# Performance work log

Hardware: AMD Instinct MI355X
Metric: run time of the kernel (lower is better)

The kernel has to match this reference:

```python
import jax, jax.numpy as jnp
import numpy as np

N_FILTERS = 1024
N_HEADS = 16


def setup_inputs() -> dict:
    key = jax.random.key(0)
    k1, k2, k3 = jax.random.split(key, 3)
    x = jax.random.normal(k1, (8, 1024, N_FILTERS), dtype=jnp.float32)
    # VarianceScaling(0.02) ~ small dense init; 0.02*sqrt(1/fan_in) scale approximated
    w_qkv = jax.random.normal(k2, (N_FILTERS, N_FILTERS * 3), dtype=jnp.float32) * (0.02 / N_FILTERS) ** 0.5
    w_out = jax.random.normal(k3, (N_FILTERS, N_FILTERS), dtype=jnp.float32) * (0.02 / N_FILTERS) ** 0.5
    return {"x": x, "w_qkv": w_qkv, "w_out": w_out}


def reference(x, w_qkv, w_out):
    b, n, c = x.shape
    h = N_HEADS
    d = c // h
    qkv = jnp.einsum('bnc,ce->bne', x, w_qkv)  # [b, n, 3c]
    q, k, v = jnp.split(qkv, 3, axis=-1)
    # b n (h d) -> b h n d
    to_heads = lambda t: t.reshape(b, n, h, d).transpose(0, 2, 1, 3)
    q, k, v = to_heads(q), to_heads(k), to_heads(v)
    scale = jnp.sqrt(jnp.asarray(c, jnp.float32))  # NOTE: sqrt(n_filters), matches source
    attn = jnp.einsum('bhnd,bhmd->bhnm', q, k) / scale
    attn = jax.nn.softmax(attn, axis=-1)
    out = jnp.einsum('bhnm,bhmd->bhnd', attn, v)
    out = out.transpose(0, 2, 1, 3).reshape(b, n, c)  # b h n d -> b n (h d)
    return jnp.einsum('bnc,co->bno', out, w_out)
```

## Files before the change

kernel.cpp:

```cpp
#include <hip/hip_runtime.h>
#include <hip/hip_bf16.h>

typedef __bf16 bf16_t;
typedef __bf16 bf16x8 __attribute__((ext_vector_type(8)));
typedef __bf16 bf16x4 __attribute__((ext_vector_type(4)));
typedef short short4v __attribute__((ext_vector_type(4)));
typedef float f32x4 __attribute__((ext_vector_type(4)));

constexpr int LD = 3072;

#define MFMA_16x16x32(a, b, c) __builtin_amdgcn_mfma_f32_16x16x32_bf16((a), (b), (c), 0, 0, 0)
#define MFMA16(a, b, c) \
  __builtin_amdgcn_mfma_f32_16x16x16bf16_1k((a), (b), (c), 0, 0, 0)

#define GLOAD_LDS16(g, l)                                               \
  __builtin_amdgcn_global_load_lds(                                     \
      (const __attribute__((address_space(1))) void*)(g),               \
      (__attribute__((address_space(3))) void*)(l), 16, 0, 0)

#define TRREAD(dst, addr, imm) \
  asm volatile("ds_read_b64_tr_b16 %0, %1 offset:" imm : "=v"(dst) : "v"(addr))

#define BAR __builtin_amdgcn_s_barrier()
#define LGKM0 do { asm volatile("s_waitcnt lgkmcnt(0)" ::: "memory"); \
                   __builtin_amdgcn_sched_barrier(0); } while (0)

__global__ __launch_bounds__(256) void prep_kernel(
    const float* __restrict__ x, bf16_t* __restrict__ x_b,
    const float* __restrict__ w_qkv, bf16_t* __restrict__ wqT,
    const float* __restrict__ w_out, bf16_t* __restrict__ woT) {
  const int blk = blockIdx.x;
  if (blk < 4096) {
    const int i = blk * 256 + threadIdx.x;
    const float4 a = reinterpret_cast<const float4*>(x)[2 * i];
    const float4 c = reinterpret_cast<const float4*>(x)[2 * i + 1];
    bf16x8 o;
    o[0] = (bf16_t)a.x; o[1] = (bf16_t)a.y; o[2] = (bf16_t)a.z; o[3] = (bf16_t)a.w;
    o[4] = (bf16_t)c.x; o[5] = (bf16_t)c.y; o[6] = (bf16_t)c.z; o[7] = (bf16_t)c.w;
    reinterpret_cast<bf16x8*>(x_b)[i] = o;
    return;
  }
  __shared__ float tile[32][33];
  const float* in; bf16_t* outp; int C, bx, by;
  if (blk < 7168) { const int i = blk - 4096; in = w_qkv; outp = wqT; C = 3072; bx = i % 96; by = i / 96; }
  else            { const int i = blk - 7168; in = w_out; outp = woT; C = 1024; bx = i & 31; by = i >> 5; }
  constexpr int R = 1024;
  const int c0 = bx * 32, r0 = by * 32;
  const int tx = threadIdx.x & 31, ty = threadIdx.x >> 5;
#pragma unroll
  for (int i = 0; i < 32; i += 8)
    tile[ty + i][tx] = in[(size_t)(r0 + ty + i) * C + (c0 + tx)];
  __syncthreads();
#pragma unroll
  for (int i = 0; i < 32; i += 8)
    outp[(size_t)(c0 + ty + i) * R + (r0 + tx)] = (bf16_t)tile[tx][ty + i];
}

__global__ __launch_bounds__(512, 2) void gemm_qkv_256(
    const bf16_t* __restrict__ A, const bf16_t* __restrict__ Bt,
    bf16_t* __restrict__ C, float q_scale) {
  constexpr int K = 1024;
  extern __shared__ char smem[];
  char* asB = smem;
  char* bsB = smem + 65536;

  const int t = threadIdx.x;
  const int lane = t & 63, wave = t >> 6;
  const int l15 = lane & 15, lg = lane >> 4;
  const int wr = wave >> 2, wc = wave & 3;

  const int bid = blockIdx.x;
  const int idx = bid >> 3;
  const int rgrp = (bid >> 1) & 3;
  const int cgrp = bid & 1;
  const int brow = (rgrp * 8 + (idx & 7)) * 256;
  const int bcol = (cgrp * 6 + (idx >> 3)) * 256;

  const int srow = t >> 3;
  const int schk = (t & 7) ^ (srow & 7);
  const bf16_t* aS = A + (size_t)(brow + srow) * K + schk * 8;
  const bf16_t* bS = Bt + (size_t)(bcol + srow) * K + schk * 8;
  const int ldst = t * 8;

#define STG_A(T, H) do {                                                      \
    const bf16_t* _s = aS + (size_t)((H) * 128) * K + (T) * 64;               \
    bf16_t* _d = (bf16_t*)(asB + ((T) & 1) * 32768 + (H) * 16384) + ldst;     \
    GLOAD_LDS16(_s, _d);                                                      \
    GLOAD_LDS16(_s + (size_t)64 * K, _d + 4096);                              \
  } while (0)
#define STG_B(T, H) do {                                                      \
    const bf16_t* _s = bS + (size_t)((H) * 128) * K + (T) * 64;               \
    bf16_t* _d = (bf16_t*)(bsB + ((T) & 1) * 32768 + (H) * 16384) + ldst;     \
    GLOAD_LDS16(_s, _d);                                                      \
    GLOAD_LDS16(_s + (size_t)64 * K, _d + 4096);                              \
  } while (0)

  const int rx = l15 & 7;
  const unsigned c0 = ((unsigned)(lg ^ rx)) << 4;
  const unsigned c1 = ((unsigned)((4 | lg) ^ rx)) << 4;
  const unsigned a_rd = (unsigned)(wr * 16384 + l15 * 128);
  const unsigned b_rd = (unsigned)((wc >> 1) * 16384 + (wc & 1) * 8192 + l15 * 128);

  f32x4 acc[8][4] = {};
  bf16x8 af[4][2], bfr[2][2];

#define RD_AF(BUF, MH) do { _Pragma("unroll")                                 \
    for (int m = 0; m < 4; ++m) {                                             \
      const char* _p = asB + (BUF) * 32768 + a_rd + ((MH) * 4 + m) * 2048;    \
      af[m][0] = *(const bf16x8*)(_p + c0);                                   \
      af[m][1] = *(const bf16x8*)(_p + c1); } } while (0)
#define RD_BF(BUF, NH) do { _Pragma("unroll")                                 \
    for (int n = 0; n < 2; ++n) {                                             \
      const char* _p = bsB + (BUF) * 32768 + b_rd + ((NH) * 2 + n) * 2048;    \
      bfr[n][0] = *(const bf16x8*)(_p + c0);                                  \
      bfr[n][1] = *(const bf16x8*)(_p + c1); } } while (0)
#define MM16(MH, NH) do {                                                     \
    __builtin_amdgcn_s_setprio(1);                                            \
    _Pragma("unroll")                                                         \
    for (int m = 0; m < 4; ++m) { _Pragma("unroll")                           \
      for (int n = 0; n < 2; ++n) {                                           \
        acc[(MH)*4+m][(NH)*2+n] =                                             \
            MFMA_16x16x32(af[m][0], bfr[n][0], acc[(MH)*4+m][(NH)*2+n]);      \
        acc[(MH)*4+m][(NH)*2+n] =                                             \
            MFMA_16x16x32(af[m][1], bfr[n][1], acc[(MH)*4+m][(NH)*2+n]); } }  \
    __builtin_amdgcn_s_setprio(0); } while (0)

  STG_A(0, 0); STG_A(0, 1); STG_B(0, 0); STG_B(0, 1); STG_A(1, 0);
  asm volatile("s_waitcnt vmcnt(2)" ::: "memory");
  BAR;

  for (int i = 0; i < 8; ++i) {
    const int T1 = 2 * i + 1, T2 = 2 * i + 2, T3 = 2 * i + 3;
    const bool pf = (i < 7);
    STG_A(T1, 1);
    RD_AF(0, 0); RD_BF(0, 0);
    BAR; LGKM0; MM16(0, 0); BAR;
    STG_B(T1, 0);
    RD_BF(0, 1);
    BAR; LGKM0; MM16(0, 1); BAR;
    STG_B(T1, 1);
    RD_AF(0, 1);
    BAR; LGKM0; MM16(1, 1); BAR;
    if (pf) STG_A(T2, 0);
    RD_BF(0, 0);
    BAR; LGKM0; MM16(1, 0);
    if (pf) asm volatile("s_waitcnt vmcnt(2)" ::: "memory");
    else    asm volatile("s_waitcnt vmcnt(0)" ::: "memory");
    BAR;
    if (pf) STG_A(T2, 1);
    RD_AF(1, 0); RD_BF(1, 0);
    BAR; LGKM0; MM16(0, 0); BAR;
    if (pf) STG_B(T2, 0);
    RD_BF(1, 1);
    BAR; LGKM0; MM16(0, 1); BAR;
    if (pf) STG_B(T2, 1);
    RD_AF(1, 1);
    BAR; LGKM0; MM16(1, 1); BAR;
    if (pf) STG_A(T3, 0);
    RD_BF(1, 0);
    BAR; LGKM0; MM16(1, 0);
    asm volatile("s_waitcnt vmcnt(2)" ::: "memory");
    BAR;
  }

  const float sc = (bcol < 1024) ? q_scale : 1.0f;
  const int crow0 = brow + wr * 128 + lg * 4;
  const int ccol0 = bcol + wc * 64 + l15;
#pragma unroll
  for (int m = 0; m < 8; ++m)
#pragma unroll
    for (int n = 0; n < 4; ++n)
#pragma unroll
      for (int r = 0; r < 4; ++r)
        C[(size_t)(crow0 + m * 16 + r) * 3072 + ccol0 + n * 16] =
            (bf16_t)(acc[m][n][r] * sc);
#undef STG_A
#undef STG_B
#undef RD_AF
#undef RD_BF
#undef MM16
}

template <typename OutT>
__global__ __launch_bounds__(512, 1) void gemm_bt_128x256(
    const bf16_t* __restrict__ A, const bf16_t* __restrict__ Bt,
    OutT* __restrict__ C, int N, int nrowblk, int q_cols, float q_scale) {
  constexpr int K = 1024;
  extern __shared__ char smem[];
  char* asB = smem;
  char* bsB = smem + 49152;

  const int t = threadIdx.x;
  const int lane = t & 63, wave = t >> 6;
  const int l15 = lane & 15, lg = lane >> 4;
  const int wr = wave >> 2, wc = wave & 3;

  const int cpx = (int)gridDim.x >> 3;
  const int bid = blockIdx.x;
  const int wg = (bid & 7) * cpx + (bid >> 3);
  const int brow = (wg % nrowblk) * 128;
  const int bcol = (wg / nrowblk) * 256;

  const int srow = t >> 3;
  const int schk = (t & 7) ^ (srow & 7);
  const bf16_t* aS = A + (size_t)(brow + srow) * K + schk * 8;
  const bf16_t* bS = Bt + (size_t)(bcol + srow) * K + schk * 8;
  const int ldst = t * 8;

#define STG_A(T, BUF) do {                                               \
    const bf16_t* _s = aS + (T) * 64;                                    \
    bf16_t* _d = (bf16_t*)(asB + (BUF) * 16384) + ldst;                  \
    GLOAD_LDS16(_s, _d);                                                 \
    GLOAD_LDS16(_s + (size_t)64 * K, _d + 4096);                         \
  } while (0)
#define STG_B(T, H, BUF) do {                                            \
    const bf16_t* _s = bS + (size_t)((H) * 128) * K + (T) * 64;          \
    bf16_t* _d = (bf16_t*)(bsB + (BUF) * 32768 + (H) * 16384) + ldst;    \
    GLOAD_LDS16(_s, _d);                                                 \
    GLOAD_LDS16(_s + (size_t)64 * K, _d + 4096);                         \
  } while (0)

  const int rx = l15 & 7;
  const unsigned c0 = ((unsigned)(lg ^ rx)) << 4;
  const unsigned c1 = ((unsigned)((4 | lg) ^ rx)) << 4;
  const unsigned a_rd = (unsigned)(wr * 8192 + l15 * 128);
  const unsigned b_rd = (unsigned)((wc >> 1) * 16384 + (wc & 1) * 8192 + l15 * 128);

  f32x4 acc[4][4] = {};
  bf16x8 af[2][2], bfr[4][2];

#define RD_AF(BUF, MH) do { _Pragma("unroll")                            \
    for (int m = 0; m < 2; ++m) {                                        \
      const char* _p = asB + (BUF) * 16384 + a_rd + ((MH) * 2 + m) * 2048; \
      af[m][0] = *(const bf16x8*)(_p + c0);                              \
      af[m][1] = *(const bf16x8*)(_p + c1); } } while (0)
#define RD_BF(BUF) do { _Pragma("unroll")                                \
    for (int n = 0; n < 4; ++n) {                                        \
      const char* _p = bsB + (BUF) * 32768 + b_rd + n * 2048;            \
      bfr[n][0] = *(const bf16x8*)(_p + c0);                             \
      bfr[n][1] = *(const bf16x8*)(_p + c1); } } while (0)
#define MM(MH) do {                                                      \
    __builtin_amdgcn_s_setprio(1);                                       \
    _Pragma("unroll")                                                    \
    for (int m = 0; m < 2; ++m) { _Pragma("unroll")                      \
      for (int n = 0; n < 4; ++n) {                                      \
        acc[(MH)*2+m][n] =                                               \
            MFMA_16x16x32(af[m][0], bfr[n][0], acc[(MH)*2+m][n]);        \
        acc[(MH)*2+m][n] =                                               \
            MFMA_16x16x32(af[m][1], bfr[n][1], acc[(MH)*2+m][n]); } }    \
    __builtin_amdgcn_s_setprio(0); } while (0)

  STG_A(0, 0); STG_B(0, 0, 0); STG_B(0, 1, 0);
  STG_A(1, 1); STG_B(1, 0, 1); STG_B(1, 1, 1);
  asm volatile("s_waitcnt vmcnt(6)" ::: "memory");
  BAR;

  int bc = 0;
  for (int T = 0; T < 16; ++T) {
    const bool pf = (T + 2 < 16);
    const int bs = (bc >= 1) ? (bc - 1) : 2;
    if (pf) { STG_A(T + 2, bs); STG_B(T + 2, 0, bs); }
    RD_AF(bc, 0);
    RD_BF(bc);
    BAR; LGKM0; MM(0); BAR;
    if (pf) STG_B(T + 2, 1, bs);
    RD_AF(bc, 1);
    BAR; LGKM0; MM(1);
    if (pf) asm volatile("s_waitcnt vmcnt(6)" ::: "memory");
    else    asm volatile("s_waitcnt vmcnt(0)" ::: "memory");
    BAR;
    bc = (bc == 2) ? 0 : bc + 1;
  }

  const float sc = (bcol < q_cols) ? q_scale : 1.0f;
  const int crow0 = brow + wr * 64 + lg * 4;
  const int ccol0 = bcol + wc * 64 + l15;
#pragma unroll
  for (int m = 0; m < 4; ++m)
#pragma unroll
    for (int n = 0; n < 4; ++n)
#pragma unroll
      for (int r = 0; r < 4; ++r)
        C[(size_t)(crow0 + m * 16 + r) * N + ccol0 + n * 16] =
            (OutT)(acc[m][n][r] * sc);
#undef STG_A
#undef STG_B
#undef RD_AF
#undef RD_BF
#undef MM
}

__device__ __forceinline__ unsigned pack_bf16_pair(float a, float b) {
  union { __hip_bfloat162 h; unsigned u; } c;
  c.h = __float22bfloat162_rn(float2{a, b});
  return c.u;
}

__global__ __launch_bounds__(256, 3) void attn_kernel(const bf16_t* __restrict__ qkv,
                                                      bf16_t* __restrict__ ctx) {
  __shared__ bf16_t Ks[2][4096];
  __shared__ bf16_t Vs[2][4096];
  const int tid = threadIdx.x, lane = tid & 63, wave = tid >> 6;
  const int l15 = lane & 15, lg = (lane >> 4) & 3;
  const int flat = blockIdx.x;
  const int xcd = flat & 7, rr = flat >> 3;
  const int qt = rr & 7;
  const int hb = xcd * 16 + (rr >> 3);
  const int h = hb & 15, b = hb >> 4;
  const size_t base = (size_t)b * 1024 * LD;
  const int qbase = qt * 128 + wave * 32;

  bf16x8 qa[2][2];
#pragma unroll
  for (int s = 0; s < 2; s++) {
    const bf16_t* qp = qkv + base + (size_t)(qbase + s * 16 + l15) * LD + h * 64 + lg * 8;
    qa[s][0] = *reinterpret_cast<const bf16x8*>(qp);
    qa[s][1] = *reinterpret_cast<const bf16x8*>(qp + 32);
  }

  const bf16_t* Kb = qkv + base + 1024 + h * 64;
  const bf16_t* Vb = qkv + base + 2048 + h * 64;

  const int krr = lane >> 3;
  const int kcc = (lane & 7) ^ krr;
  const bf16_t* ksrc0 = Kb + (size_t)(wave * 16 + krr) * LD + kcc * 8;
  const bf16_t* ksrc1 = ksrc0 + (size_t)8 * LD;

  const int vd0 = (lane & 1) * 8 + wave * 16;
  const int vkv = ((lane >> 1) & 3) + ((lane >> 3) & 3) * 4 + (lane >> 5) * 16;
  const bf16_t* vsrc0 = Vb + (size_t)vkv * LD + vd0;
  const bf16_t* vsrc1 = vsrc0 + (size_t)32 * LD;

  bf16_t* ksb = &Ks[0][0];
  bf16_t* vsb = &Vs[0][0];
  const char* ksr = (const char*)&Ks[0][0];
  const unsigned vs_byte =
      (unsigned)(size_t)(__attribute__((address_space(3))) void*)(&Vs[0][0]);
  const unsigned tr_lane = vs_byte + lane * 8;

  const int rx7 = l15 & 7;
  const unsigned kb0 = (unsigned)(l15 * 128 + ((lg ^ rx7) << 4));
  const unsigned kb1 = (unsigned)(l15 * 128 + (((4 | lg) ^ rx7) << 4));

  short4v ones4;
#pragma unroll
  for (int j = 0; j < 4; j++) {
    union { bf16_t f; short s; } cu; cu.f = (bf16_t)1.0f;
    ones4[j] = cu.s;
  }

  f32x4 dn[2] = {};
  f32x4 oacc[2][4] = {};

  GLOAD_LDS16(ksrc0, ksb + wave * 1024);
  GLOAD_LDS16(ksrc1, ksb + wave * 1024 + 512);
  GLOAD_LDS16(vsrc0, vsb + wave * 1024);
  GLOAD_LDS16(vsrc1, vsb + wave * 1024 + 512);
  ksrc0 += (size_t)64 * LD; ksrc1 += (size_t)64 * LD;
  vsrc0 += (size_t)64 * LD; vsrc1 += (size_t)64 * LD;
  __syncthreads();

#pragma unroll 4
  for (int t = 0; t < 16; t++) {
    const int cur = t & 1;
    if (t < 15) {
      bf16_t* kd = ksb + (cur ^ 1) * 4096 + wave * 1024;
      bf16_t* vd = vsb + (cur ^ 1) * 4096 + wave * 1024;
      GLOAD_LDS16(ksrc0, kd);
      GLOAD_LDS16(ksrc1, kd + 512);
      GLOAD_LDS16(vsrc0, vd);
      GLOAD_LDS16(vsrc1, vd + 512);
      ksrc0 += (size_t)64 * LD; ksrc1 += (size_t)64 * LD;
      vsrc0 += (size_t)64 * LD; vsrc1 += (size_t)64 * LD;
    }

    f32x4 sacc[2][4] = {};
    const char* kt = ksr + cur * 8192;
    __builtin_amdgcn_s_setprio(1);
#pragma unroll
    for (int tt = 0; tt < 4; tt++) {
      const bf16x8 k0 = *reinterpret_cast<const bf16x8*>(kt + tt * 2048 + kb0);
      const bf16x8 k1 = *reinterpret_cast<const bf16x8*>(kt + tt * 2048 + kb1);
      sacc[0][tt] = MFMA_16x16x32(k0, qa[0][0], sacc[0][tt]);
      sacc[0][tt] = MFMA_16x16x32(k1, qa[0][1], sacc[0][tt]);
      sacc[1][tt] = MFMA_16x16x32(k0, qa[1][0], sacc[1][tt]);
      sacc[1][tt] = MFMA_16x16x32(k1, qa[1][1], sacc[1][tt]);
    }
    __builtin_amdgcn_s_setprio(0);

    const unsigned ta = tr_lane + (unsigned)cur * 8192;
    short4v tl0, th0, tl2, th2, tl4, th4, tl6, th6;
    TRREAD(tl0, ta, "0");    TRREAD(th0, ta, "512");
    TRREAD(tl2, ta, "2048"); TRREAD(th2, ta, "2560");
    TRREAD(tl4, ta, "4096"); TRREAD(th4, ta, "4608");
    TRREAD(tl6, ta, "6144"); TRREAD(th6, ta, "6656");
    __builtin_amdgcn_sched_barrier(0);

    unsigned pu[16];
#pragma unroll
    for (int tt = 0; tt < 4; tt++) {
      const float a0 = __builtin_exp2f(sacc[0][tt][0]);
      const float a1 = __builtin_exp2f(sacc[0][tt][1]);
      const float a2 = __builtin_exp2f(sacc[0][tt][2]);
      const float a3 = __builtin_exp2f(sacc[0][tt][3]);
      pu[(tt >> 1) * 4 + (tt & 1) * 2 + 0] = pack_bf16_pair(a0, a1);
      pu[(tt >> 1) * 4 + (tt & 1) * 2 + 1] = pack_bf16_pair(a2, a3);
      const float b0 = __builtin_exp2f(sacc[1][tt][0]);
      const float b1 = __builtin_exp2f(sacc[1][tt][1]);
      const float b2 = __builtin_exp2f(sacc[1][tt][2]);
      const float b3 = __builtin_exp2f(sacc[1][tt][3]);
      pu[8 + (tt >> 1) * 4 + (tt & 1) * 2 + 0] = pack_bf16_pair(b0, b1);
      pu[8 + (tt >> 1) * 4 + (tt & 1) * 2 + 1] = pack_bf16_pair(b2, b3);
    }
    short4v paL[2][2], paH[2][2];
#pragma unroll
    for (int s = 0; s < 2; s++)
#pragma unroll
      for (int ks = 0; ks < 2; ks++) {
        paL[s][ks] = *reinterpret_cast<short4v*>(&pu[s * 8 + ks * 4]);
        paH[s][ks] = *reinterpret_cast<short4v*>(&pu[s * 8 + ks * 4 + 2]);
      }

#pragma unroll
    for (int s = 0; s < 2; s++)
#pragma unroll
      for (int ks = 0; ks < 2; ks++) {
        dn[s] = MFMA16(paL[s][ks], ones4, dn[s]);
        dn[s] = MFMA16(paH[s][ks], ones4, dn[s]);
      }

    short4v tl1, th1, tl3, th3, tl5, th5, tl7, th7;
    TRREAD(tl1, ta, "1024"); TRREAD(th1, ta, "1536");
    TRREAD(tl3, ta, "3072"); TRREAD(th3, ta, "3584");
    TRREAD(tl5, ta, "5120"); TRREAD(th5, ta, "5632");
    TRREAD(tl7, ta, "7168"); TRREAD(th7, ta, "7680");

    asm volatile("s_waitcnt lgkmcnt(8)" ::: "memory");
    __builtin_amdgcn_sched_barrier(0);
    __builtin_amdgcn_s_setprio(1);
#pragma unroll
    for (int s = 0; s < 2; s++) {
      oacc[s][0] = MFMA16(paL[s][0], tl0, oacc[s][0]);
      oacc[s][0] = MFMA16(paH[s][0], th0, oacc[s][0]);
      oacc[s][1] = MFMA16(paL[s][0], tl2, oacc[s][1]);
      oacc[s][1] = MFMA16(paH[s][0], th2, oacc[s][1]);
      oacc[s][2] = MFMA16(paL[s][0], tl4, oacc[s][2]);
      oacc[s][2] = MFMA16(paH[s][0], th4, oacc[s][2]);
      oacc[s][3] = MFMA16(paL[s][0], tl6, oacc[s][3]);
      oacc[s][3] = MFMA16(paH[s][0], th6, oacc[s][3]);
    }
    __builtin_amdgcn_s_setprio(0);

    asm volatile("s_waitcnt lgkmcnt(0)" ::: "memory");
    __builtin_amdgcn_sched_barrier(0);
    __builtin_amdgcn_s_setprio(1);
#pragma unroll
    for (int s = 0; s < 2; s++) {
      oacc[s][0] = MFMA16(paL[s][1], tl1, oacc[s][0]);
      oacc[s][0] = MFMA16(paH[s][1], th1, oacc[s][0]);
      oacc[s][1] = MFMA16(paL[s][1], tl3, oacc[s][1]);
      oacc[s][1] = MFMA16(paH[s][1], th3, oacc[s][1]);
      oacc[s][2] = MFMA16(paL[s][1], tl5, oacc[s][2]);
      oacc[s][2] = MFMA16(paH[s][1], th5, oacc[s][2]);
      oacc[s][3] = MFMA16(paL[s][1], tl7, oacc[s][3]);
      oacc[s][3] = MFMA16(paH[s][1], th7, oacc[s][3]);
    }
    __builtin_amdgcn_s_setprio(0);

    __syncthreads();
  }

#pragma unroll
  for (int s = 0; s < 2; s++) {
#pragma unroll
    for (int r = 0; r < 4; r++) {
      const float inv = 1.0f / dn[s][r];
      const size_t row = (size_t)(b * 1024 + qbase + s * 16 + lg * 4 + r);
#pragma unroll
      for (int dt = 0; dt < 4; dt++)
        ctx[row * 1024 + h * 64 + dt * 16 + l15] = (bf16_t)(oacc[s][dt][r] * inv);
    }
  }
}

extern "C" void kernel_launch(void* const* d_in, const int* in_sizes, int n_in,
                              void* d_out, int out_size, void* d_ws, size_t ws_size,
                              hipStream_t stream) {
  (void)in_sizes; (void)n_in; (void)out_size; (void)ws_size;
  const float* x = (const float*)d_in[0];
  const float* w_qkv = (const float*)d_in[1];
  const float* w_out = (const float*)d_in[2];
  float* out = (float*)d_out;
  char* ws = (char*)d_ws;

  bf16_t* x_b   = (bf16_t*)(ws);
  bf16_t* qkv_b = (bf16_t*)(ws + (size_t)(16 << 20));
  bf16_t* wqT   = (bf16_t*)(ws + (size_t)(64 << 20));
  bf16_t* woT   = (bf16_t*)(ws + (size_t)(70 << 20));
  bf16_t* ctx_b = (bf16_t*)(ws + (size_t)(72 << 20));

  const float qsc = 0.045084220027780106f;

  prep_kernel<<<8192, 256, 0, stream>>>(x, x_b, w_qkv, wqT, w_out, woT);
  gemm_qkv_256<<<384, 512, 131072, stream>>>(x_b, wqT, qkv_b, qsc);
  attn_kernel<<<1024, 256, 0, stream>>>(qkv_b, ctx_b);
  gemm_bt_128x256<float><<<256, 512, 147456, stream>>>(
      ctx_b, woT, out, 1024, 64, 0, 1.0f);
}
```

Measured before the change: 155.7 us.

## Process two query tiles per attention block to reuse K/V tiles

Each attention workgroup now handles 256 query rows (two 128-row sub-tiles per wave set) instead of 128, so every K/V tile staged in LDS is used for twice as many queries and global K/V traffic halves. The grid shrinks from 1024 to 512 blocks and the launch bound drops to 2 waves per SIMD to make room for the doubled accumulators and Q fragments. All V transpose reads are now issued up front and waited on once. The cost is higher register pressure, lower occupancy and fewer blocks to spread across CUs.

```diff
diff --git a/kernel.cpp b/kernel.cpp
--- a/kernel.cpp
+++ b/kernel.cpp
@@ -296,7 +296,7 @@
   return c.u;
 }
 
-__global__ __launch_bounds__(256, 3) void attn_kernel(const bf16_t* __restrict__ qkv,
+__global__ __launch_bounds__(256, 2) void attn_kernel(const bf16_t* __restrict__ qkv,
                                                       bf16_t* __restrict__ ctx) {
   __shared__ bf16_t Ks[2][4096];
   __shared__ bf16_t Vs[2][4096];
@@ -304,19 +304,22 @@
   const int l15 = lane & 15, lg = (lane >> 4) & 3;
   const int flat = blockIdx.x;
   const int xcd = flat & 7, rr = flat >> 3;
-  const int qt = rr & 7;
-  const int hb = xcd * 16 + (rr >> 3);
+  const int qt2 = rr & 3;
+  const int hb = xcd * 16 + (rr >> 2);
   const int h = hb & 15, b = hb >> 4;
   const size_t base = (size_t)b * 1024 * LD;
-  const int qbase = qt * 128 + wave * 32;
-
-  bf16x8 qa[2][2];
-#pragma unroll
-  for (int s = 0; s < 2; s++) {
-    const bf16_t* qp = qkv + base + (size_t)(qbase + s * 16 + l15) * LD + h * 64 + lg * 8;
-    qa[s][0] = *reinterpret_cast<const bf16x8*>(qp);
-    qa[s][1] = *reinterpret_cast<const bf16x8*>(qp + 32);
-  }
+  const int qbase = qt2 * 256 + wave * 32;
+
+  bf16x8 qa[2][2][2];
+#pragma unroll
+  for (int s2 = 0; s2 < 2; s2++)
+#pragma unroll
+    for (int s = 0; s < 2; s++) {
+      const bf16_t* qp =
+          qkv + base + (size_t)(qbase + s2 * 128 + s * 16 + l15) * LD + h * 64 + lg * 8;
+      qa[s2][s][0] = *reinterpret_cast<const bf16x8*>(qp);
+      qa[s2][s][1] = *reinterpret_cast<const bf16x8*>(qp + 32);
+    }
 
   const bf16_t* Kb = qkv + base + 1024 + h * 64;
   const bf16_t* Vb = qkv + base + 2048 + h * 64;
@@ -349,8 +352,8 @@
     ones4[j] = cu.s;
   }
 
-  f32x4 dn[2] = {};
-  f32x4 oacc[2][4] = {};
+  f32x4 dn[2][2] = {};
+  f32x4 oacc[2][2][4] = {};
 
   GLOAD_LDS16(ksrc0, ksb + wave * 1024);
   GLOAD_LDS16(ksrc1, ksb + wave * 1024 + 512);
@@ -360,7 +363,7 @@
   vsrc0 += (size_t)64 * LD; vsrc1 += (size_t)64 * LD;
   __syncthreads();
 
-#pragma unroll 4
+#pragma unroll 2
   for (int t = 0; t < 16; t++) {
     const int cur = t & 1;
     if (t < 15) {
@@ -374,113 +377,141 @@
       vsrc0 += (size_t)64 * LD; vsrc1 += (size_t)64 * LD;
     }
 
-    f32x4 sacc[2][4] = {};
     const char* kt = ksr + cur * 8192;
+    const unsigned ta = tr_lane + (unsigned)cur * 8192;
+    short4v paL[2][2][2], paH[2][2][2];
+
+    f32x4 sacc0[2][4] = {};
     __builtin_amdgcn_s_setprio(1);
 #pragma unroll
     for (int tt = 0; tt < 4; tt++) {
       const bf16x8 k0 = *reinterpret_cast<const bf16x8*>(kt + tt * 2048 + kb0);
       const bf16x8 k1 = *reinterpret_cast<const bf16x8*>(kt + tt * 2048 + kb1);
-      sacc[0][tt] = MFMA_16x16x32(k0, qa[0][0], sacc[0][tt]);
-      sacc[0][tt] = MFMA_16x16x32(k1, qa[0][1], sacc[0][tt]);
-      sacc[1][tt] = MFMA_16x16x32(k0, qa[1][0], sacc[1][tt]);
-      sacc[1][tt] = MFMA_16x16x32(k1, qa[1][1], sacc[1][tt]);
+      sacc0[0][tt] = MFMA_16x16x32(k0, qa[0][0][0], sacc0[0][tt]);
+      sacc0[0][tt] = MFMA_16x16x32(k1, qa[0][0][1], sacc0[0][tt]);
+      sacc0[1][tt] = MFMA_16x16x32(k0, qa[0][1][0], sacc0[1][tt]);
+      sacc0[1][tt] = MFMA_16x16x32(k1, qa[0][1][1], sacc0[1][tt]);
     }
     __builtin_amdgcn_s_setprio(0);
 
-    const unsigned ta = tr_lane + (unsigned)cur * 8192;
-    short4v tl0, th0, tl2, th2, tl4, th4, tl6, th6;
+    short4v tl0, th0, tl1, th1, tl2, th2, tl3, th3;
+    short4v tl4, th4, tl5, th5, tl6, th6, tl7, th7;
     TRREAD(tl0, ta, "0");    TRREAD(th0, ta, "512");
+    TRREAD(tl1, ta, "1024"); TRREAD(th1, ta, "1536");
     TRREAD(tl2, ta, "2048"); TRREAD(th2, ta, "2560");
+    TRREAD(tl3, ta, "3072"); TRREAD(th3, ta, "3584");
     TRREAD(tl4, ta, "4096"); TRREAD(th4, ta, "4608");
+    TRREAD(tl5, ta, "5120"); TRREAD(th5, ta, "5632");
     TRREAD(tl6, ta, "6144"); TRREAD(th6, ta, "6656");
+    TRREAD(tl7, ta, "7168"); TRREAD(th7, ta, "7680");
     __builtin_amdgcn_sched_barrier(0);
 
-    unsigned pu[16];
+    {
+      unsigned pu[16];
+#pragma unroll
+      for (int tt = 0; tt < 4; tt++) {
+#pragma unroll
+        for (int s = 0; s < 2; s++) {
+          const float p0 = __builtin_exp2f(sacc0[s][tt][0]);
+          const float p1 = __builtin_exp2f(sacc0[s][tt][1]);
+          const float p2 = __builtin_exp2f(sacc0[s][tt][2]);
+          const float p3 = __builtin_exp2f(sacc0[s][tt][3]);
+          pu[s * 8 + (tt >> 1) * 4 + (tt & 1) * 2 + 0] = pack_bf16_pair(p0, p1);
+          pu[s * 8 + (tt >> 1) * 4 + (tt & 1) * 2 + 1] = pack_bf16_pair(p2, p3);
+        }
+      }
+#pragma unroll
+      for (int s = 0; s < 2; s++)
+#pragma unroll
+        for (int ks = 0; ks < 2; ks++) {
+          paL[0][s][ks] = *reinterpret_cast<short4v*>(&pu[s * 8 + ks * 4]);
+          paH[0][s][ks] = *reinterpret_cast<short4v*>(&pu[s * 8 + ks * 4 + 2]);
+          dn[0][s] = MFMA16(paL[0][s][ks], ones4, dn[0][s]);
+          dn[0][s] = MFMA16(paH[0][s][ks], ones4, dn[0][s]);
+        }
+    }
+
+    f32x4 sacc1[2][4] = {};
+    __builtin_amdgcn_s_setprio(1);
 #pragma unroll
     for (int tt = 0; tt < 4; tt++) {
-      const float a0 = __builtin_exp2f(sacc[0][tt][0]);
-      const float a1 = __builtin_exp2f(sacc[0][tt][1]);
-      const float a2 = __builtin_exp2f(sacc[0][tt][2]);
-      const float a3 = __builtin_exp2f(sacc[0][tt][3]);
-      pu[(tt >> 1) * 4 + (tt & 1) * 2 + 0] = pack_bf16_pair(a0, a1);
-      pu[(tt >> 1) * 4 + (tt & 1) * 2 + 1] = pack_bf16_pair(a2, a3);
-      const float b0 = __builtin_exp2f(sacc[1][tt][0]);
-      const float b1 = __builtin_exp2f(sacc[1][tt][1]);
-      const float b2 = __builtin_exp2f(sacc[1][tt][2]);
-      const float b3 = __builtin_exp2f(sacc[1][tt][3]);
-      pu[8 + (tt >> 1) * 4 + (tt & 1) * 2 + 0] = pack_bf16_pair(b0, b1);
-      pu[8 + (tt >> 1) * 4 + (tt & 1) * 2 + 1] = pack_bf16_pair(b2, b3);
-    }
-    short4v paL[2][2], paH[2][2];
-#pragma unroll
-    for (int s = 0; s < 2; s++)
-#pragma unroll
-      for (int ks = 0; ks < 2; ks++) {
-        paL[s][ks] = *reinterpret_cast<short4v*>(&pu[s * 8 + ks * 4]);
-        paH[s][ks] = *reinterpret_cast<short4v*>(&pu[s * 8 + ks * 4 + 2]);
-      }
-
-#pragma unroll
-    for (int s = 0; s < 2; s++)
-#pragma unroll
-      for (int ks = 0; ks < 2; ks++) {
-        dn[s] = MFMA16(paL[s][ks], ones4, dn[s]);
-        dn[s] = MFMA16(paH[s][ks], ones4, dn[s]);
-      }
-
-    short4v tl1, th1, tl3, th3, tl5, th5, tl7, th7;
-    TRREAD(tl1, ta, "1024"); TRREAD(th1, ta, "1536");
-    TRREAD(tl3, ta, "3072"); TRREAD(th3, ta, "3584");
-    TRREAD(tl5, ta, "5120"); TRREAD(th5, ta, "5632");
-    TRREAD(tl7, ta, "7168"); TRREAD(th7, ta, "7680");
-
-    asm volatile("s_waitcnt lgkmcnt(8)" ::: "memory");
-    __builtin_amdgcn_sched_barrier(0);
-    __builtin_amdgcn_s_setprio(1);
-#pragma unroll
-    for (int s = 0; s < 2; s++) {
-      oacc[s][0] = MFMA16(paL[s][0], tl0, oacc[s][0]);
-      oacc[s][0] = MFMA16(paH[s][0], th0, oacc[s][0]);
-      oacc[s][1] = MFMA16(paL[s][0], tl2, oacc[s][1]);
-      oacc[s][1] = MFMA16(paH[s][0], th2, oacc[s][1]);
-      oacc[s][2] = MFMA16(paL[s][0], tl4, oacc[s][2]);
-      oacc[s][2] = MFMA16(paH[s][0], th4, oacc[s][2]);
-      oacc[s][3] = MFMA16(paL[s][0], tl6, oacc[s][3]);
-      oacc[s][3] = MFMA16(paH[s][0], th6, oacc[s][3]);
+      const bf16x8 k0 = *reinterpret_cast<const bf16x8*>(kt + tt * 2048 + kb0);
+      const bf16x8 k1 = *reinterpret_cast<const bf16x8*>(kt + tt * 2048 + kb1);
+      sacc1[0][tt] = MFMA_16x16x32(k0, qa[1][0][0], sacc1[0][tt]);
+      sacc1[0][tt] = MFMA_16x16x32(k1, qa[1][0][1], sacc1[0][tt]);
+      sacc1[1][tt] = MFMA_16x16x32(k0, qa[1][1][0], sacc1[1][tt]);
+      sacc1[1][tt] = MFMA_16x16x32(k1, qa[1][1][1], sacc1[1][tt]);
     }
     __builtin_amdgcn_s_setprio(0);
 
-    asm volatile("s_waitcnt lgkmcnt(0)" ::: "memory");
-    __builtin_amdgcn_sched_barrier(0);
+    {
+      unsigned pu[16];
+#pragma unroll
+      for (int tt = 0; tt < 4; tt++) {
+#pragma unroll
+        for (int s = 0; s < 2; s++) {
+          const float p0 = __builtin_exp2f(sacc1[s][tt][0]);
+          const float p1 = __builtin_exp2f(sacc1[s][tt][1]);
+          const float p2 = __builtin_exp2f(sacc1[s][tt][2]);
+          const float p3 = __builtin_exp2f(sacc1[s][tt][3]);
+          pu[s * 8 + (tt >> 1) * 4 + (tt & 1) * 2 + 0] = pack_bf16_pair(p0, p1);
+          pu[s * 8 + (tt >> 1) * 4 + (tt & 1) * 2 + 1] = pack_bf16_pair(p2, p3);
+        }
+      }
+#pragma unroll
+      for (int s = 0; s < 2; s++)
+#pragma unroll
+        for (int ks = 0; ks < 2; ks++) {
+          paL[1][s][ks] = *reinterpret_cast<short4v*>(&pu[s * 8 + ks * 4]);
+          paH[1][s][ks] = *reinterpret_cast<short4v*>(&pu[s * 8 + ks * 4 + 2]);
+          dn[1][s] = MFMA16(paL[1][s][ks], ones4, dn[1][s]);
+          dn[1][s] = MFMA16(paH[1][s][ks], ones4, dn[1][s]);
+        }
+    }
+
+    LGKM0;
+
     __builtin_amdgcn_s_setprio(1);
 #pragma unroll
-    for (int s = 0; s < 2; s++) {
-      oacc[s][0] = MFMA16(paL[s][1], tl1, oacc[s][0]);
-      oacc[s][0] = MFMA16(paH[s][1], th1, oacc[s][0]);
-      oacc[s][1] = MFMA16(paL[s][1], tl3, oacc[s][1]);
-      oacc[s][1] = MFMA16(paH[s][1], th3, oacc[s][1]);
-      oacc[s][2] = MFMA16(paL[s][1], tl5, oacc[s][2]);
-      oacc[s][2] = MFMA16(paH[s][1], th5, oacc[s][2]);
-      oacc[s][3] = MFMA16(paL[s][1], tl7, oacc[s][3]);
-      oacc[s][3] = MFMA16(paH[s][1], th7, oacc[s][3]);
-    }
+    for (int s2 = 0; s2 < 2; s2++)
+#pragma unroll
+      for (int s = 0; s < 2; s++) {
+        oacc[s2][s][0] = MFMA16(paL[s2][s][0], tl0, oacc[s2][s][0]);
+        oacc[s2][s][0] = MFMA16(paH[s2][s][0], th0, oacc[s2][s][0]);
+        oacc[s2][s][0] = MFMA16(paL[s2][s][1], tl1, oacc[s2][s][0]);
+        oacc[s2][s][0] = MFMA16(paH[s2][s][1], th1, oacc[s2][s][0]);
+        oacc[s2][s][1] = MFMA16(paL[s2][s][0], tl2, oacc[s2][s][1]);
+        oacc[s2][s][1] = MFMA16(paH[s2][s][0], th2, oacc[s2][s][1]);
+        oacc[s2][s][1] = MFMA16(paL[s2][s][1], tl3, oacc[s2][s][1]);
+        oacc[s2][s][1] = MFMA16(paH[s2][s][1], th3, oacc[s2][s][1]);
+        oacc[s2][s][2] = MFMA16(paL[s2][s][0], tl4, oacc[s2][s][2]);
+        oacc[s2][s][2] = MFMA16(paH[s2][s][0], th4, oacc[s2][s][2]);
+        oacc[s2][s][2] = MFMA16(paL[s2][s][1], tl5, oacc[s2][s][2]);
+        oacc[s2][s][2] = MFMA16(paH[s2][s][1], th5, oacc[s2][s][2]);
+        oacc[s2][s][3] = MFMA16(paL[s2][s][0], tl6, oacc[s2][s][3]);
+        oacc[s2][s][3] = MFMA16(paH[s2][s][0], th6, oacc[s2][s][3]);
+        oacc[s2][s][3] = MFMA16(paL[s2][s][1], tl7, oacc[s2][s][3]);
+        oacc[s2][s][3] = MFMA16(paH[s2][s][1], th7, oacc[s2][s][3]);
+      }
     __builtin_amdgcn_s_setprio(0);
 
     __syncthreads();
   }
 
 #pragma unroll
-  for (int s = 0; s < 2; s++) {
-#pragma unroll
-    for (int r = 0; r < 4; r++) {
-      const float inv = 1.0f / dn[s][r];
-      const size_t row = (size_t)(b * 1024 + qbase + s * 16 + lg * 4 + r);
-#pragma unroll
-      for (int dt = 0; dt < 4; dt++)
-        ctx[row * 1024 + h * 64 + dt * 16 + l15] = (bf16_t)(oacc[s][dt][r] * inv);
-    }
-  }
+  for (int s2 = 0; s2 < 2; s2++)
+#pragma unroll
+    for (int s = 0; s < 2; s++)
+#pragma unroll
+      for (int r = 0; r < 4; r++) {
+        const float inv = 1.0f / dn[s2][s][r];
+        const size_t row =
+            (size_t)(b * 1024 + qbase + s2 * 128 + s * 16 + lg * 4 + r);
+#pragma unroll
+        for (int dt = 0; dt < 4; dt++)
+          ctx[row * 1024 + h * 64 + dt * 16 + l15] =
+              (bf16_t)(oacc[s2][s][dt][r] * inv);
+      }
 }
 
 extern "C" void kernel_launch(void* const* d_in, const int* in_sizes, int n_in,
@@ -503,7 +534,7 @@
 
   prep_kernel<<<8192, 256, 0, stream>>>(x, x_b, w_qkv, wqT, w_out, woT);
   gemm_qkv_256<<<384, 512, 131072, stream>>>(x_b, wqT, qkv_b, qsc);
-  attn_kernel<<<1024, 256, 0, stream>>>(qkv_b, ctx_b);
+  attn_kernel<<<512, 256, 0, stream>>>(qkv_b, ctx_b);
   gemm_bt_128x256<float><<<256, 512, 147456, stream>>>(
       ctx_b, woT, out, 1024, 64, 0, 1.0f);
 }
```

Result: no change. 157.7 us (+1.3%).
